# Kernel tuning notes

Hardware: AMD Instinct MI355X
Metric: run time of the kernel (lower is better)

## Reference

```python
import jax, jax.numpy as jnp
import numpy as np
import math

PHI = (1 + math.sqrt(5)) / 2
PI = math.pi
B, N, T, D, H = 2, 16, 512, 512, 8
DH = D // H
HALF = DH // 2
FF = int(D * PHI)  # 828
DC = D
PR_EPS = 1e-8
LN_EPS = 1e-5


def _ln(x, g, b):
    # x: (B,N,T,D); g,b: (N,D)
    mu = x.mean(axis=-1, keepdims=True)
    var = ((x - mu) ** 2).mean(axis=-1, keepdims=True)
    return (x - mu) * jax.lax.rsqrt(var + LN_EPS) * g[None, :, None, :] + b[None, :, None, :]


def _phase_resonance(a, b):
    # a, b: (B, N, D) in fp32; adjacent feature pairs = (re, im)
    pairs = a.shape[-1] // 2
    def to_phase(x):
        x2 = x.reshape(*x.shape[:-1], pairs, 2)
        return jnp.arctan2(x2[..., 1] + PR_EPS, x2[..., 0] + PR_EPS)
    ta, tb = to_phase(a), to_phase(b)
    delta = ta[..., :, None, :] - tb[..., None, :, :]  # (B, N, N, pairs)
    return jnp.cos(delta).mean(axis=-1)                # (B, N, N) in [-1, 1]


def setup_inputs():
    key = jax.random.key(0)
    ks = iter(jax.random.split(key, 24))
    w = lambda shape: jax.random.normal(next(ks), shape, jnp.float32) * 0.02
    return {
        'x': jax.random.normal(next(ks), (B, N, T, D), jnp.float32),
        'gate_w': w((N, D)),
        'gate_b': jnp.full((N,), 2.0, jnp.float32),  # torch init: bias=2.0
        'ln1_g': jnp.ones((N, D), jnp.float32),
        'ln1_b': jnp.zeros((N, D), jnp.float32),
        'wq': w((N, D, D)), 'wk': w((N, D, D)), 'wv': w((N, D, D)), 'wo': w((N, D, D)),
        'phase_angles': jnp.tile(jnp.linspace(0.0, PI, H, dtype=jnp.float32), (N, 1)),
        'ln2_g': jnp.ones((N, D), jnp.float32),
        'ln2_b': jnp.zeros((N, D), jnp.float32),
        'up_w': w((N, D, FF)), 'up_b': jnp.zeros((N, FF), jnp.float32),
        'down_w': w((N, FF, D)), 'down_b': jnp.zeros((N, D), jnp.float32),
        'commit_w': w((N, D)), 'commit_b': jnp.zeros((N,), jnp.float32),
        'center_w': w((N, D, DC)), 'center_b': jnp.zeros((N, DC), jnp.float32),
        'field_in_w': w((D, D)),
        'field_out_w': w((D, D)),
        'conductance': jnp.float32(1.0),
    }


def reference(x, gate_w, gate_b, ln1_g, ln1_b, wq, wk, wv, wo, phase_angles,
              ln2_g, ln2_b, up_w, up_b, down_w, down_b, commit_w, commit_b,
              center_w, center_b, field_in_w, field_out_w, conductance):
    # ---- BinaryAperture (straight-through binary gate) ----
    logits = jnp.einsum('bntd,nd->bnt', x, gate_w) + gate_b[None, :, None]
    prob = jax.nn.sigmoid(logits)  # temperature = 1.0
    hard = (prob > 0.5).astype(x.dtype)
    gate = (hard + prob - jax.lax.stop_gradient(prob))[..., None]  # (B,N,T,1)

    # ---- Field: phase-rotated, gated attention (scores forced to fp32) ----
    h = _ln(x, ln1_g, ln1_b)
    def proj(wm):
        z = jnp.einsum('bntd,nde->bnte', h, wm)
        return z.reshape(B, N, T, H, DH).transpose(0, 1, 3, 2, 4)  # (B,N,H,T,DH)
    Q, K, V = proj(wq), proj(wk), proj(wv)
    cos_a = jnp.cos(phase_angles)[None, :, :, None, None]  # (1,N,H,1,1)
    sin_a = jnp.sin(phase_angles)[None, :, :, None, None]
    def rot(Z):
        re, im = Z[..., :HALF], Z[..., HALF:2 * HALF]
        return jnp.concatenate([re * cos_a - im * sin_a, re * sin_a + im * cos_a], axis=-1)
    Q, K = rot(Q), rot(K)
    ge = gate[:, :, None]  # (B,N,1,T,1) broadcast over heads
    Q = Q * ge
    K = K * ge
    scores = jnp.einsum('bnhtd,bnhsd->bnhts', Q.astype(jnp.float32), K.astype(jnp.float32)) / math.sqrt(DH)
    attn = jax.nn.softmax(scores, axis=-1).astype(V.dtype)
    field = jnp.einsum('bnhts,bnhsd->bnhtd', attn, V)
    field = field.transpose(0, 1, 3, 2, 4).reshape(B, N, T, D)
    field = jnp.einsum('bntd,nde->bnte', field, wo) * gate
    x = x + field

    # ---- Boundary: golden-ratio FFN gated by commit * gate ----
    h2 = _ln(x, ln2_g, ln2_b)
    up = jax.nn.gelu(jnp.einsum('bntd,ndf->bntf', h2, up_w) + up_b[None, :, None], approximate=False)
    ff = jnp.einsum('bntf,nfd->bntd', up, down_w) + down_b[None, :, None]
    center_pool = x.mean(axis=2)  # (B,N,D) (pooled pre-FFN, as in torch)
    commit = jax.nn.sigmoid(jnp.einsum('bnd,nd->bn', center_pool, commit_w) + commit_b[None])  # (B,N)
    x = x + commit[..., None, None] * gate * ff
    center = jnp.tanh(jnp.einsum('bnd,nde->bne', center_pool, center_w) + center_b[None])  # (B,N,DC)

    # ---- SharedField: phase-resonance coupling across the N nodes ----
    node_gates = commit[..., None]  # (B,N,1)
    transmitted = center * node_gates
    h_res = jnp.einsum('bnd,de->bne', center, field_in_w).astype(jnp.float32)
    r_acc = _phase_resonance(h_res, h_res)  # (B,N,N); r_acc None -> r_acc_new = r_instant
    h_tx = jnp.einsum('bnd,de->bne', transmitted, field_in_w)
    recv = conductance * jnp.einsum('bmn,bnd->bmd', r_acc.astype(x.dtype), h_tx)
    field_signal = jnp.einsum('bnd,de->bne', recv, field_out_w)  # (B,N,D)

    # each node's boundary receives the field signal
    return x + field_signal[:, :, None, :]
```

## Files before the change

### kernel.cpp

```cpp
#include <hip/hip_runtime.h>

typedef unsigned short u16;
typedef __attribute__((ext_vector_type(8))) short short8;
typedef __attribute__((ext_vector_type(4))) float f32x4;

#define B_ 2
#define N_ 16
#define T_ 512
#define D_ 512
#define H_ 8
#define DH_ 64
#define HALF_ 32
#define FF_ 828
#define FFP_ 832
#define DC_ 512
#define LN_EPS 1e-5f
#define PR_EPS 1e-8f
#define NEG_INF (-3.0e38f)

__device__ __forceinline__ float b2f(u16 u) { return __uint_as_float(((unsigned)u) << 16); }
__device__ __forceinline__ u16 f2b(float f) {
  unsigned x = __float_as_uint(f);
  return (u16)((x + 0x7fffu + ((x >> 16) & 1u)) >> 16);
}
__device__ __forceinline__ float gelu_exact(float z) {
  return 0.5f * z * (1.f + erff(z * 0.70710678118654752f));
}

typedef __attribute__((address_space(1))) const unsigned GASu;
typedef __attribute__((address_space(3))) unsigned LASu;
__device__ __forceinline__ void gload_lds16(const void* g, void* l) {
  __builtin_amdgcn_global_load_lds((GASu*)g, (LASu*)l, 16, 0, 0);
}

__global__ __launch_bounds__(256) void ln_gate_kernel(
    const float* __restrict__ xsrc,
    const float* __restrict__ gate_w, const float* __restrict__ gate_b,
    const float* __restrict__ lng, const float* __restrict__ lnb,
    float* __restrict__ gate_out, u16* __restrict__ h_out, int do_gate) {
  __shared__ float redA[4], redB[4], redC[4];
  int bnt = blockIdx.x;
  int n = (bnt / T_) % N_;
  int tid = threadIdx.x;
  int lane = tid & 63, wave = tid >> 6;
  const float* xr = xsrc + (size_t)bnt * D_;
  float x0 = xr[tid], x1 = xr[tid + 256];
  float s = x0 + x1;
  #pragma unroll
  for (int off = 32; off > 0; off >>= 1) s += __shfl_xor(s, off);
  if (lane == 0) redA[wave] = s;
  if (do_gate) {
    float t = x0 * gate_w[n * D_ + tid] + x1 * gate_w[n * D_ + tid + 256];
    #pragma unroll
    for (int off = 32; off > 0; off >>= 1) t += __shfl_xor(t, off);
    if (lane == 0) redC[wave] = t;
  }
  __syncthreads();
  float mu = (redA[0] + redA[1] + redA[2] + redA[3]) * (1.f / D_);
  float d0 = x0 - mu, d1 = x1 - mu;
  float v = d0 * d0 + d1 * d1;
  #pragma unroll
  for (int off = 32; off > 0; off >>= 1) v += __shfl_xor(v, off);
  if (lane == 0) redB[wave] = v;
  __syncthreads();
  float rstd = rsqrtf((redB[0] + redB[1] + redB[2] + redB[3]) * (1.f / D_) + LN_EPS);
  if (do_gate && tid == 0)
    gate_out[bnt] = (redC[0] + redC[1] + redC[2] + redC[3] + gate_b[n] > 0.f) ? 1.f : 0.f;
  size_t o = (size_t)bnt * D_;
  h_out[o + tid]       = f2b(d0 * rstd * lng[n * D_ + tid]       + lnb[n * D_ + tid]);
  h_out[o + tid + 256] = f2b(d1 * rstd * lng[n * D_ + tid + 256] + lnb[n * D_ + tid + 256]);
}

__global__ __launch_bounds__(256) void wconv_kernel(
    const float* __restrict__ W, u16* __restrict__ Wt, int Kd, int E, int Kpad) {
  __shared__ u16 tile[32][33];
  int e0 = blockIdx.x * 32, k0 = blockIdx.y * 32, n = blockIdx.z;
  const float* Wb = W + (size_t)n * Kd * E;
  u16* Wtb = Wt + (size_t)n * E * Kpad;
  int r = threadIdx.x >> 3, c4 = (threadIdx.x & 7) * 4;
  int kk = k0 + r;
  if (kk < Kd) {
    if (e0 + c4 + 3 < E) {
      float4 w4 = *(const float4*)(Wb + (size_t)kk * E + e0 + c4);
      tile[r][c4 + 0] = f2b(w4.x); tile[r][c4 + 1] = f2b(w4.y);
      tile[r][c4 + 2] = f2b(w4.z); tile[r][c4 + 3] = f2b(w4.w);
    } else {
      #pragma unroll
      for (int j = 0; j < 4; ++j) {
        int ee = e0 + c4 + j;
        tile[r][c4 + j] = (ee < E) ? f2b(Wb[(size_t)kk * E + ee]) : (u16)0;
      }
    }
  } else {
    #pragma unroll
    for (int j = 0; j < 4; ++j) tile[r][c4 + j] = 0;
  }
  __syncthreads();
  int ee = e0 + r;
  if (ee < E) {
    u16* dst = Wtb + (size_t)ee * Kpad + k0 + c4;
    if (k0 + c4 + 3 < Kpad) {
      ushort4 o;
      o.x = tile[c4 + 0][r]; o.y = tile[c4 + 1][r];
      o.z = tile[c4 + 2][r]; o.w = tile[c4 + 3][r];
      *(ushort4*)dst = o;
    } else {
      #pragma unroll
      for (int j = 0; j < 4; ++j) if (k0 + c4 + j < Kpad) dst[j] = tile[c4 + j][r];
    }
  }
}

__global__ __launch_bounds__(256) void vtrans_kernel(const u16* __restrict__ V, u16* __restrict__ Vt) {
  __shared__ u16 tile[32][36];
  int tt0 = blockIdx.x * 32;
  int dd0 = blockIdx.y * 32;
  int bh = blockIdx.z;
  int bn = bh >> 3, h = bh & 7;
  const u16* src = V + (size_t)bn * T_ * D_ + h * DH_;
  int r = threadIdx.x >> 3, c4 = (threadIdx.x & 7) * 4;
  *(ushort4*)&tile[r][c4] = *(const ushort4*)(src + (size_t)(tt0 + r) * D_ + dd0 + c4);
  __syncthreads();
  u16* dst = Vt + ((size_t)bh * DH_ + dd0 + r) * T_ + tt0 + c4;
  ushort4 o;
  o.x = tile[c4 + 0][r]; o.y = tile[c4 + 1][r];
  o.z = tile[c4 + 2][r]; o.w = tile[c4 + 3][r];
  *(ushort4*)dst = o;
}

#define BM 128
#define BN 128
#define BK 64
__global__ __launch_bounds__(256) void gemm_mfma_kernel(
    const u16* __restrict__ In,
    const float* __restrict__ W0, const float* __restrict__ W1, const float* __restrict__ W2,
    const u16* __restrict__ Wt0, const u16* __restrict__ Wt1, const u16* __restrict__ Wt2,
    u16* __restrict__ O0, u16* __restrict__ O1, u16* __restrict__ O2,
    float* __restrict__ OutF,
    int Kd, int KdW, int E, int Es, int mode,
    const float* __restrict__ bias,
    const float* __restrict__ xres, const float* __restrict__ gate) {
  __shared__ __align__(16) u16 As[BM * BK];
  __shared__ __align__(16) u16 Bs[BN * BK];
  int z = blockIdx.z;
  int bn = z & 31, proj = z >> 5;
  int n = bn & (N_ - 1);
  const float* W = (proj == 0) ? W0 : ((proj == 1) ? W1 : W2);
  const u16* Wt = (proj == 0) ? Wt0 : ((proj == 1) ? Wt1 : Wt2);
  u16* Out = (proj == 0) ? O0 : ((proj == 1) ? O1 : O2);
  int e0 = blockIdx.x * BN, t0 = blockIdx.y * BM;
  int tid = threadIdx.x;
  int lane = tid & 63, wave = tid >> 6;
  int m_off = (wave & 1) * 64, n_off = (wave >> 1) * 64;
  int ml = lane & 15, quad = lane >> 4;
  const u16* Inb = In + (size_t)bn * T_ * Kd;
  const float* Wb = W ? W + (size_t)n * (size_t)KdW * E : nullptr;
  const u16* Wtb = Wt ? Wt + (size_t)n * E * Kd : nullptr;

  int lrow = lane >> 3;
  int lchunk = ((lane & 7) ^ lrow) * 8;

  f32x4 acc[4][4] = {};

  int ksteps = (Kd + BK - 1) / BK;
  for (int ks = 0; ks < ksteps; ++ks) {
    int k0 = ks * BK;
    if (Wtb) {
      #pragma unroll
      for (int it = 0; it < 4; ++it) {
        int r0 = wave * 32 + it * 8;
        gload_lds16(Inb + (size_t)(t0 + r0 + lrow) * Kd + k0 + lchunk, &As[r0 * BK]);
        gload_lds16(Wtb + (size_t)(e0 + r0 + lrow) * Kd + k0 + lchunk, &Bs[r0 * BK]);
      }
    } else {
      #pragma unroll
      for (int it = 0; it < 4; ++it) {
        int cid = tid * 4 + it;
        int r = cid >> 3, cp = cid & 7;
        int clog = cp ^ (r & 7);
        int kg = k0 + clog * 8;
        u16* dst = &As[r * BK + cp * 8];
        const u16* src = Inb + (size_t)(t0 + r) * Kd + kg;
        if (kg + 8 <= Kd) {
          *(short8*)dst = *(const short8*)src;
        } else {
          #pragma unroll
          for (int xx = 0; xx < 8; ++xx) dst[xx] = (kg + xx < Kd) ? src[xx] : (u16)0;
        }
        int eg = e0 + r;
        u16* bdst = &Bs[r * BK + cp * 8];
        #pragma unroll
        for (int xx = 0; xx < 8; ++xx)
          bdst[xx] = (kg + xx < KdW && eg < E) ? f2b(Wb[(size_t)(kg + xx) * E + eg]) : (u16)0;
      }
    }
    __syncthreads();
    #pragma unroll
    for (int kst = 0; kst < 2; ++kst) {
      int so = ((kst * 4 + quad) ^ (ml & 7)) * 8;
      short8 a[4], b[4];
      #pragma unroll
      for (int i = 0; i < 4; ++i)
        a[i] = *(const short8*)&As[(m_off + i * 16 + ml) * BK + so];
      #pragma unroll
      for (int j = 0; j < 4; ++j)
        b[j] = *(const short8*)&Bs[(n_off + j * 16 + ml) * BK + so];
      #pragma unroll
      for (int i = 0; i < 4; ++i)
        #pragma unroll
        for (int j = 0; j < 4; ++j)
          acc[i][j] = __builtin_amdgcn_mfma_f32_16x16x32_bf16(a[i], b[j], acc[i][j], 0, 0, 0);
    }
    __syncthreads();
  }

  #pragma unroll
  for (int j = 0; j < 4; ++j) {
    int eg = e0 + n_off + j * 16 + ml;
    if (eg >= Es) continue;
    #pragma unroll
    for (int i = 0; i < 4; ++i) {
      #pragma unroll
      for (int r = 0; r < 4; ++r) {
        int tg = t0 + m_off + i * 16 + quad * 4 + r;
        float v = acc[i][j][r];
        size_t o = (size_t)bn * T_ * Es + (size_t)tg * Es + eg;
        if (mode == 0) {
          Out[o] = f2b(v);
        } else if (mode == 1) {
          float g = gate[(size_t)bn * T_ + tg];
          OutF[o] = xres[o] + v * g;
        } else if (mode == 2) {
          Out[o] = (eg < E) ? f2b(gelu_exact(v + bias[(size_t)n * E + eg])) : (u16)0;
        } else {
          Out[o] = f2b(v + bias[(size_t)n * E + eg]);
        }
      }
    }
  }
}

__global__ __launch_bounds__(256) void rot_gate_kernel(
    u16* __restrict__ q, u16* __restrict__ k,
    const float* __restrict__ phase, const float* __restrict__ gate) {
  long long i = (long long)blockIdx.x * 256 + threadIdx.x;
  int c = (int)(i & 31);
  int h = (int)((i >> 5) & 7);
  int t = (int)((i >> 8) & 511);
  int bn = (int)(i >> 17);
  int n = bn & (N_ - 1);
  float a = phase[n * H_ + h];
  float ca = cosf(a), sa = sinf(a);
  float g = gate[(size_t)bn * T_ + t];
  size_t base = ((size_t)bn * T_ + t) * D_ + h * DH_;
  float qr = b2f(q[base + c]), qi = b2f(q[base + c + HALF_]);
  u16 a0 = f2b((qr * ca - qi * sa) * g);
  u16 a1 = f2b((qr * sa + qi * ca) * g);
  q[base + c]         = f2b(b2f(a0) * 0.125f);
  q[base + c + HALF_] = f2b(b2f(a1) * 0.125f);
  float kr = b2f(k[base + c]), ki = b2f(k[base + c + HALF_]);
  k[base + c]         = f2b((kr * ca - ki * sa) * g);
  k[base + c + HALF_] = f2b((kr * sa + ki * ca) * g);
}

#define ATS 72
__global__ __launch_bounds__(256) void attn_kernel(
    const u16* __restrict__ Q, const u16* __restrict__ K, const u16* __restrict__ V,
    const u16* __restrict__ Vt, u16* __restrict__ O) {
  __shared__ __align__(16) u16 Qs[64 * ATS];
  __shared__ __align__(16) u16 Ks[64 * ATS];
  __shared__ __align__(16) u16 Vs[64 * ATS];
  __shared__ __align__(16) u16 Ps[64 * ATS];
  int qt = blockIdx.x, h = blockIdx.y, bn = blockIdx.z;
  int tid = threadIdx.x;
  int lane = tid & 63, wave = tid >> 6;
  int ml = lane & 15, quad = lane >> 4;
  int t0 = qt * 64;
  size_t rowbase = (size_t)bn * T_ * D_ + (size_t)h * DH_;
  int r = tid >> 2;
  int c = (tid & 3) * 16;

  {
    const u16* src = Q + rowbase + (size_t)(t0 + r) * D_ + c;
    *(short8*)&Qs[r * ATS + c]     = *(const short8*)(src);
    *(short8*)&Qs[r * ATS + c + 8] = *(const short8*)(src + 8);
  }
  const u16* ksrc = K + rowbase + (size_t)r * D_ + c;
  const u16* vsrc = Vt ? (Vt + ((size_t)(bn * H_ + h) * DH_ + r) * T_ + c) : nullptr;

  float m_[4], l_[4];
  f32x4 acco[4] = {};
  #pragma unroll
  for (int rr = 0; rr < 4; ++rr) { m_[rr] = NEG_INF; l_[rr] = 0.f; }

  for (int sc = 0; sc < 8; ++sc) {
    int s0 = sc * 64;
    {
      const u16* kp = ksrc + (size_t)s0 * D_;
      *(short8*)&Ks[r * ATS + c]     = *(const short8*)(kp);
      *(short8*)&Ks[r * ATS + c + 8] = *(const short8*)(kp + 8);
    }
    if (Vt) {
      const u16* vp = vsrc + s0;
      *(short8*)&Vs[r * ATS + c]     = *(const short8*)(vp);
      *(short8*)&Vs[r * ATS + c + 8] = *(const short8*)(vp + 8);
    } else {
      int sw = wave * 16;
      const u16* src = V + rowbase + (size_t)(s0 + sw) * D_ + lane;
      short8 v0, v1;
      #pragma unroll
      for (int rr = 0; rr < 8; ++rr) ((u16*)&v0)[rr] = src[(size_t)rr * D_];
      #pragma unroll
      for (int rr = 0; rr < 8; ++rr) ((u16*)&v1)[rr] = src[(size_t)(rr + 8) * D_];
      *(short8*)&Vs[lane * ATS + sw]     = v0;
      *(short8*)&Vs[lane * ATS + sw + 8] = v1;
    }
    __syncthreads();

    f32x4 s4[4] = {};
    #pragma unroll
    for (int kst = 0; kst < 2; ++kst) {
      short8 a = *(const short8*)&Qs[(wave * 16 + ml) * ATS + kst * 32 + quad * 8];
      #pragma unroll
      for (int j = 0; j < 4; ++j) {
        short8 b = *(const short8*)&Ks[(j * 16 + ml) * ATS + kst * 32 + quad * 8];
        s4[j] = __builtin_amdgcn_mfma_f32_16x16x32_bf16(a, b, s4[j], 0, 0, 0);
      }
    }

    #pragma unroll
    for (int rr = 0; rr < 4; ++rr) {
      float cm = fmaxf(fmaxf(s4[0][rr], s4[1][rr]), fmaxf(s4[2][rr], s4[3][rr]));
      #pragma unroll
      for (int off = 1; off < 16; off <<= 1) cm = fmaxf(cm, __shfl_xor(cm, off));
      if (cm > m_[rr]) {
        float al = __expf(m_[rr] - cm);
        l_[rr] *= al;
        #pragma unroll
        for (int jd = 0; jd < 4; ++jd) acco[jd][rr] *= al;
        m_[rr] = cm;
      }
      u16 q0 = f2b(__expf(s4[0][rr] - m_[rr])), q1 = f2b(__expf(s4[1][rr] - m_[rr]));
      u16 q2 = f2b(__expf(s4[2][rr] - m_[rr])), q3 = f2b(__expf(s4[3][rr] - m_[rr]));
      float rs = b2f(q0) + b2f(q1) + b2f(q2) + b2f(q3);
      #pragma unroll
      for (int off = 1; off < 16; off <<= 1) rs += __shfl_xor(rs, off);
      l_[rr] += rs;
      int trow = wave * 16 + quad * 4 + rr;
      Ps[trow * ATS + 0 * 16 + ml] = q0;
      Ps[trow * ATS + 1 * 16 + ml] = q1;
      Ps[trow * ATS + 2 * 16 + ml] = q2;
      Ps[trow * ATS + 3 * 16 + ml] = q3;
    }

    #pragma unroll
    for (int sst = 0; sst < 2; ++sst) {
      short8 a = *(const short8*)&Ps[(wave * 16 + ml) * ATS + sst * 32 + quad * 8];
      #pragma unroll
      for (int jd = 0; jd < 4; ++jd) {
        short8 b = *(const short8*)&Vs[(jd * 16 + ml) * ATS + sst * 32 + quad * 8];
        acco[jd] = __builtin_amdgcn_mfma_f32_16x16x32_bf16(a, b, acco[jd], 0, 0, 0);
      }
    }
    __syncthreads();
  }

  #pragma unroll
  for (int rr = 0; rr < 4; ++rr) {
    float inv = 1.f / l_[rr];
    int trow = t0 + wave * 16 + quad * 4 + rr;
    #pragma unroll
    for (int jd = 0; jd < 4; ++jd)
      O[rowbase + (size_t)trow * D_ + jd * 16 + ml] = f2b(acco[jd][rr] * inv);
  }
}

__global__ __launch_bounds__(256) void pool1_kernel(const float* __restrict__ x2, float* __restrict__ part) {
  int tc = blockIdx.x & 15, bn = blockIdx.x >> 4;
  int d = threadIdx.x;
  const float* base = x2 + ((size_t)bn * T_ + tc * 32) * D_;
  float s0 = 0.f, s1 = 0.f;
  for (int t = 0; t < 32; ++t) {
    s0 += base[(size_t)t * D_ + d];
    s1 += base[(size_t)t * D_ + d + 256];
  }
  float* p = part + ((size_t)bn * 16 + tc) * D_;
  p[d] = s0; p[d + 256] = s1;
}
__global__ __launch_bounds__(256) void pool2_kernel(const float* __restrict__ part, float* __restrict__ cp) {
  int bn = blockIdx.x;
  int d = threadIdx.x;
  float s0 = 0.f, s1 = 0.f;
  for (int tc = 0; tc < 16; ++tc) {
    s0 += part[((size_t)bn * 16 + tc) * D_ + d];
    s1 += part[((size_t)bn * 16 + tc) * D_ + d + 256];
  }
  cp[(size_t)bn * D_ + d]       = s0 * (1.f / T_);
  cp[(size_t)bn * D_ + d + 256] = s1 * (1.f / T_);
}

__global__ __launch_bounds__(256) void commit_center_kernel(
    const float* __restrict__ cp, const float* __restrict__ commit_w, const float* __restrict__ commit_b,
    const float* __restrict__ center_w, const float* __restrict__ center_b,
    float* __restrict__ commit, float* __restrict__ center) {
  __shared__ float cps[512];
  __shared__ float red[256];
  int bn = blockIdx.x, n = bn % N_, tid = threadIdx.x;
  cps[tid] = cp[(size_t)bn * D_ + tid];
  cps[tid + 256] = cp[(size_t)bn * D_ + tid + 256];
  __syncthreads();
  red[tid] = cps[tid] * commit_w[n * D_ + tid] + cps[tid + 256] * commit_w[n * D_ + tid + 256];
  __syncthreads();
  for (int s = 128; s > 0; s >>= 1) { if (tid < s) red[tid] += red[tid + s]; __syncthreads(); }
  if (tid == 0) commit[bn] = 1.f / (1.f + expf(-(red[0] + commit_b[n])));
  #pragma unroll
  for (int eo = 0; eo < 2; ++eo) {
    int e = eo * 256 + tid;
    float acc = center_b[(size_t)n * DC_ + e];
    for (int d = 0; d < D_; ++d) acc = fmaf(cps[d], center_w[((size_t)n * D_ + d) * DC_ + e], acc);
    center[(size_t)bn * DC_ + e] = tanhf(acc);
  }
}

__global__ __launch_bounds__(256) void matvec_kernel(
    const float* __restrict__ inp, const float* __restrict__ Wm, float* __restrict__ outp) {
  __shared__ float s[512];
  int bn = blockIdx.x, tid = threadIdx.x;
  s[tid] = inp[(size_t)bn * D_ + tid];
  s[tid + 256] = inp[(size_t)bn * D_ + tid + 256];
  __syncthreads();
  #pragma unroll
  for (int eo = 0; eo < 2; ++eo) {
    int e = eo * 256 + tid;
    float acc = 0.f;
    for (int d = 0; d < D_; ++d) acc = fmaf(s[d], Wm[(size_t)d * D_ + e], acc);
    outp[(size_t)bn * D_ + e] = acc;
  }
}

__global__ __launch_bounds__(256) void uv_kernel(
    const float* __restrict__ hres, float* __restrict__ u, float* __restrict__ v) {
  int i = blockIdx.x * 256 + threadIdx.x;
  float xr = hres[2 * i] + PR_EPS;
  float yi = hres[2 * i + 1] + PR_EPS;
  float r = sqrtf(xr * xr + yi * yi);
  u[i] = xr / r; v[i] = yi / r;
}

__global__ __launch_bounds__(256) void racc_kernel(
    const float* __restrict__ u, const float* __restrict__ v, float* __restrict__ ra) {
  int b = blockIdx.x, tid = threadIdx.x;
  int mm = tid >> 4, nn = tid & 15;
  const float* ub = u + (size_t)b * N_ * 256;
  const float* vb = v + (size_t)b * N_ * 256;
  float acc = 0.f;
  for (int p = 0; p < 256; ++p)
    acc += ub[mm * 256 + p] * ub[nn * 256 + p] + vb[mm * 256 + p] * vb[nn * 256 + p];
  ra[(size_t)b * N_ * N_ + mm * N_ + nn] = acc * (1.f / 256.f);
}

__global__ __launch_bounds__(256) void recv_kernel(
    const float* __restrict__ ra, const float* __restrict__ commit,
    const float* __restrict__ hres, const float* __restrict__ cond, float* __restrict__ recv) {
  int bn = blockIdx.x, b = bn / N_, mm = bn % N_, tid = threadIdx.x;
  float c = cond[0];
  #pragma unroll
  for (int eo = 0; eo < 2; ++eo) {
    int d = eo * 256 + tid;
    float acc = 0.f;
    for (int nn = 0; nn < N_; ++nn)
      acc += ra[(size_t)b * N_ * N_ + mm * N_ + nn] * commit[b * N_ + nn] *
             hres[((size_t)b * N_ + nn) * D_ + d];
    recv[(size_t)bn * D_ + d] = c * acc;
  }
}

__global__ __launch_bounds__(256) void final_kernel(
    const float* __restrict__ x2, const float* __restrict__ commit,
    const float* __restrict__ gate, const u16* __restrict__ ff,
    const float* __restrict__ fs, float* __restrict__ out) {
  long long i4 = (long long)blockIdx.x * 256 + threadIdx.x;
  long long base = i4 * 4;
  int d = (int)(base & (D_ - 1));
  int t = (int)((base >> 9) & (T_ - 1));
  int bn = (int)(base >> 18);
  float cg = commit[bn] * gate[(size_t)bn * T_ + t];
  float4 xv = *(const float4*)(x2 + base);
  ushort4 fv = *(const ushort4*)(ff + base);
  float4 sv = *(const float4*)(fs + (size_t)bn * D_ + d);
  float4 r;
  r.x = xv.x + cg * b2f(fv.x) + sv.x;
  r.y = xv.y + cg * b2f(fv.y) + sv.y;
  r.z = xv.z + cg * b2f(fv.z) + sv.z;
  r.w = xv.w + cg * b2f(fv.w) + sv.w;
  *(float4*)(out + base) = r;
}

extern "C" void kernel_launch(void* const* d_in, const int* in_sizes, int n_in,
                              void* d_out, int out_size, void* d_ws, size_t ws_size,
                              hipStream_t stream) {
  (void)in_sizes; (void)n_in; (void)out_size;
  const float* x          = (const float*)d_in[0];
  const float* gate_w     = (const float*)d_in[1];
  const float* gate_b     = (const float*)d_in[2];
  const float* ln1_g      = (const float*)d_in[3];
  const float* ln1_b      = (const float*)d_in[4];
  const float* wq         = (const float*)d_in[5];
  const float* wk         = (const float*)d_in[6];
  const float* wv         = (const float*)d_in[7];
  const float* wo         = (const float*)d_in[8];
  const float* phase      = (const float*)d_in[9];
  const float* ln2_g      = (const float*)d_in[10];
  const float* ln2_b      = (const float*)d_in[11];
  const float* up_w       = (const float*)d_in[12];
  const float* up_b       = (const float*)d_in[13];
  const float* down_w     = (const float*)d_in[14];
  const float* down_b     = (const float*)d_in[15];
  const float* commit_w   = (const float*)d_in[16];
  const float* commit_b   = (const float*)d_in[17];
  const float* center_w   = (const float*)d_in[18];
  const float* center_b   = (const float*)d_in[19];
  const float* field_in_w = (const float*)d_in[20];
  const float* field_out_w= (const float*)d_in[21];
  const float* cond       = (const float*)d_in[22];

  const long long BNTD = 8388608LL;
  u16* w16 = (u16*)d_ws;
  u16* R0 = w16;
  u16* R1 = w16 + BNTD;
  u16* R2 = w16 + 2 * BNTD;
  u16* R3 = w16 + 3 * BNTD;
  float* sm   = (float*)(w16 + 4 * BNTD);
  float* gate   = sm;
  float* cp     = sm + 16384;
  float* center = sm + 2 * 16384;
  float* hres   = sm + 3 * 16384;
  float* uu     = sm + 4 * 16384;
  float* vv     = uu + 8192;
  float* ra     = vv + 8192;
  float* recvb  = ra + 512;
  float* fsig   = recvb + 16384;
  float* commit = fsig + 16384;
  float* part   = sm + 115232;
  float* x2 = (float*)d_out;

  const size_t WSQ = (size_t)N_ * 512 * 512;
  const size_t WUPu = (size_t)N_ * 828 * 512;
  const size_t WUPd = (size_t)N_ * 512 * 832;
  u16* wtbase = (u16*)(sm + 115232 + 262144);
  u16* wtq = wtbase;
  u16* wtk = wtq + WSQ;
  u16* wtv = wtk + WSQ;
  u16* wto = wtv + WSQ;
  u16* wtu = wto + WSQ;
  u16* wtd = wtu + WUPu;
  u16* vtb = wtd + WUPd;
  size_t needed = (size_t)((char*)(vtb + BNTD) - (char*)d_ws);
  bool use_wt = ws_size >= needed;

  ln_gate_kernel<<<16384, 256, 0, stream>>>(x, gate_w, gate_b, ln1_g, ln1_b, gate, R0, 1);

  if (use_wt) {
    wconv_kernel<<<dim3(16, 16, 16), 256, 0, stream>>>(wq, wtq, 512, 512, 512);
    wconv_kernel<<<dim3(16, 16, 16), 256, 0, stream>>>(wk, wtk, 512, 512, 512);
    wconv_kernel<<<dim3(16, 16, 16), 256, 0, stream>>>(wv, wtv, 512, 512, 512);
    wconv_kernel<<<dim3(16, 16, 16), 256, 0, stream>>>(wo, wto, 512, 512, 512);
    wconv_kernel<<<dim3(26, 16, 16), 256, 0, stream>>>(up_w, wtu, 512, 828, 512);
    wconv_kernel<<<dim3(16, 26, 16), 256, 0, stream>>>(down_w, wtd, 828, 512, 832);
  }
  const u16* pq = use_wt ? wtq : nullptr;
  const u16* pk = use_wt ? wtk : nullptr;
  const u16* pv = use_wt ? wtv : nullptr;
  const u16* po = use_wt ? wto : nullptr;
  const u16* pu = use_wt ? wtu : nullptr;
  const u16* pd = use_wt ? wtd : nullptr;

  gemm_mfma_kernel<<<dim3(4, 4, 96), 256, 0, stream>>>(
      R0, wq, wk, wv, pq, pk, pv, R1, R2, R3, nullptr,
      512, 512, 512, 512, 0, nullptr, nullptr, nullptr);
  rot_gate_kernel<<<16384, 256, 0, stream>>>(R1, R2, phase, gate);
  if (use_wt) vtrans_kernel<<<dim3(16, 2, 256), 256, 0, stream>>>(R3, vtb);
  attn_kernel<<<dim3(8, 8, 32), 256, 0, stream>>>(R1, R2, R3, use_wt ? vtb : nullptr, R0);
  gemm_mfma_kernel<<<dim3(4, 4, 32), 256, 0, stream>>>(
      R0, wo, nullptr, nullptr, po, nullptr, nullptr, nullptr, nullptr, nullptr, x2,
      512, 512, 512, 512, 1, nullptr, x, gate);
  ln_gate_kernel<<<16384, 256, 0, stream>>>(x2, nullptr, nullptr, ln2_g, ln2_b, nullptr, R1, 0);
  gemm_mfma_kernel<<<dim3(7, 4, 32), 256, 0, stream>>>(
      R1, up_w, nullptr, nullptr, pu, nullptr, nullptr, R2, nullptr, nullptr, nullptr,
      512, 512, 828, 832, 2, up_b, nullptr, nullptr);
  gemm_mfma_kernel<<<dim3(4, 4, 32), 256, 0, stream>>>(
      R2, down_w, nullptr, nullptr, pd, nullptr, nullptr, R0, nullptr, nullptr, nullptr,
      832, 828, 512, 512, 3, down_b, nullptr, nullptr);
  pool1_kernel<<<512, 256, 0, stream>>>(x2, part);
  pool2_kernel<<<32, 256, 0, stream>>>(part, cp);
  commit_center_kernel<<<32, 256, 0, stream>>>(cp, commit_w, commit_b, center_w, center_b, commit, center);
  matvec_kernel<<<32, 256, 0, stream>>>(center, field_in_w, hres);
  uv_kernel<<<32, 256, 0, stream>>>(hres, uu, vv);
  racc_kernel<<<2, 256, 0, stream>>>(uu, vv, ra);
  recv_kernel<<<32, 256, 0, stream>>>(ra, commit, hres, cond, recvb);
  matvec_kernel<<<32, 256, 0, stream>>>(recvb, field_out_w, fsig);
  final_kernel<<<8192, 256, 0, stream>>>(x2, commit, gate, R0, fsig, x2);
}
```

Measured before the change: 780.4 us.

## Fuse rotary phase gating into QKV GEMM epilogue and remap blocks per XCD

The separate rot_gate kernel is removed and its rotation, gating and q-scaling are applied in the QKV GEMM epilogue. Each wave's 64 output columns form one head, so the re/im halves are acc[j] and acc[j+2]. This avoids a full read-modify-write pass over Q and K. All GEMM launches also move to a 1D grid that keeps each z-slice's tiles on one XCD (blockIdx & 7), to improve L2 reuse of the weights and inputs. The bf16 rounding sequence is kept so results match, at the cost of a larger epilogue.

```diff
diff --git a/kernel.cpp b/kernel.cpp
--- a/kernel.cpp
+++ b/kernel.cpp
@@ -139,16 +139,22 @@
     float* __restrict__ OutF,
     int Kd, int KdW, int E, int Es, int mode,
     const float* __restrict__ bias,
-    const float* __restrict__ xres, const float* __restrict__ gate) {
+    const float* __restrict__ xres, const float* __restrict__ gate,
+    const float* __restrict__ phase, int doRot,
+    int xdim, int nXY, int zPerXcd) {
   __shared__ __align__(16) u16 As[BM * BK];
   __shared__ __align__(16) u16 Bs[BN * BK];
-  int z = blockIdx.z;
+  int L = blockIdx.x;
+  int xcd = L & 7, slot = L >> 3;
+  int zloc = slot / nXY, xy = slot - zloc * nXY;
+  int z = xcd * zPerXcd + zloc;
+  int bx = xy % xdim, by = xy / xdim;
   int bn = z & 31, proj = z >> 5;
   int n = bn & (N_ - 1);
   const float* W = (proj == 0) ? W0 : ((proj == 1) ? W1 : W2);
   const u16* Wt = (proj == 0) ? Wt0 : ((proj == 1) ? Wt1 : Wt2);
   u16* Out = (proj == 0) ? O0 : ((proj == 1) ? O1 : O2);
-  int e0 = blockIdx.x * BN, t0 = blockIdx.y * BM;
+  int e0 = bx * BN, t0 = by * BM;
   int tid = threadIdx.x;
   int lane = tid & 63, wave = tid >> 6;
   int m_off = (wave & 1) * 64, n_off = (wave >> 1) * 64;
@@ -214,53 +220,57 @@
     __syncthreads();
   }
 
-  #pragma unroll
-  for (int j = 0; j < 4; ++j) {
-    int eg = e0 + n_off + j * 16 + ml;
-    if (eg >= Es) continue;
+  int rmode = doRot ? ((proj == 0) ? 2 : ((proj == 1) ? 1 : 0)) : 0;
+  if (rmode) {
+    int h = (e0 + n_off) >> 6;
+    float ang = phase[n * H_ + h];
+    float ca = cosf(ang), sa = sinf(ang);
     #pragma unroll
     for (int i = 0; i < 4; ++i) {
       #pragma unroll
       for (int r = 0; r < 4; ++r) {
         int tg = t0 + m_off + i * 16 + quad * 4 + r;
-        float v = acc[i][j][r];
-        size_t o = (size_t)bn * T_ * Es + (size_t)tg * Es + eg;
-        if (mode == 0) {
-          Out[o] = f2b(v);
-        } else if (mode == 1) {
-          float g = gate[(size_t)bn * T_ + tg];
-          OutF[o] = xres[o] + v * g;
-        } else if (mode == 2) {
-          Out[o] = (eg < E) ? f2b(gelu_exact(v + bias[(size_t)n * E + eg])) : (u16)0;
-        } else {
-          Out[o] = f2b(v + bias[(size_t)n * E + eg]);
+        float g = gate[(size_t)bn * T_ + tg];
+        #pragma unroll
+        for (int j = 0; j < 2; ++j) {
+          int eg = e0 + n_off + j * 16 + ml;
+          size_t o = (size_t)bn * T_ * Es + (size_t)tg * Es + eg;
+          float re = b2f(f2b(acc[i][j][r]));
+          float im = b2f(f2b(acc[i][j + 2][r]));
+          u16 a0 = f2b((re * ca - im * sa) * g);
+          u16 a1 = f2b((re * sa + im * ca) * g);
+          if (rmode == 2) { a0 = f2b(b2f(a0) * 0.125f); a1 = f2b(b2f(a1) * 0.125f); }
+          Out[o] = a0;
+          Out[o + 32] = a1;
         }
       }
     }
-  }
-}
-
-__global__ __launch_bounds__(256) void rot_gate_kernel(
-    u16* __restrict__ q, u16* __restrict__ k,
-    const float* __restrict__ phase, const float* __restrict__ gate) {
-  long long i = (long long)blockIdx.x * 256 + threadIdx.x;
-  int c = (int)(i & 31);
-  int h = (int)((i >> 5) & 7);
-  int t = (int)((i >> 8) & 511);
-  int bn = (int)(i >> 17);
-  int n = bn & (N_ - 1);
-  float a = phase[n * H_ + h];
-  float ca = cosf(a), sa = sinf(a);
-  float g = gate[(size_t)bn * T_ + t];
-  size_t base = ((size_t)bn * T_ + t) * D_ + h * DH_;
-  float qr = b2f(q[base + c]), qi = b2f(q[base + c + HALF_]);
-  u16 a0 = f2b((qr * ca - qi * sa) * g);
-  u16 a1 = f2b((qr * sa + qi * ca) * g);
-  q[base + c]         = f2b(b2f(a0) * 0.125f);
-  q[base + c + HALF_] = f2b(b2f(a1) * 0.125f);
-  float kr = b2f(k[base + c]), ki = b2f(k[base + c + HALF_]);
-  k[base + c]         = f2b((kr * ca - ki * sa) * g);
-  k[base + c + HALF_] = f2b((kr * sa + ki * ca) * g);
+  } else {
+    #pragma unroll
+    for (int j = 0; j < 4; ++j) {
+      int eg = e0 + n_off + j * 16 + ml;
+      if (eg >= Es) continue;
+      #pragma unroll
+      for (int i = 0; i < 4; ++i) {
+        #pragma unroll
+        for (int r = 0; r < 4; ++r) {
+          int tg = t0 + m_off + i * 16 + quad * 4 + r;
+          float v = acc[i][j][r];
+          size_t o = (size_t)bn * T_ * Es + (size_t)tg * Es + eg;
+          if (mode == 0) {
+            Out[o] = f2b(v);
+          } else if (mode == 1) {
+            float g = gate[(size_t)bn * T_ + tg];
+            OutF[o] = xres[o] + v * g;
+          } else if (mode == 2) {
+            Out[o] = (eg < E) ? f2b(gelu_exact(v + bias[(size_t)n * E + eg])) : (u16)0;
+          } else {
+            Out[o] = f2b(v + bias[(size_t)n * E + eg]);
+          }
+        }
+      }
+    }
+  }
 }
 
 #define ATS 72
@@ -575,22 +585,21 @@
   const u16* pu = use_wt ? wtu : nullptr;
   const u16* pd = use_wt ? wtd : nullptr;
 
-  gemm_mfma_kernel<<<dim3(4, 4, 96), 256, 0, stream>>>(
+  gemm_mfma_kernel<<<1536, 256, 0, stream>>>(
       R0, wq, wk, wv, pq, pk, pv, R1, R2, R3, nullptr,
-      512, 512, 512, 512, 0, nullptr, nullptr, nullptr);
-  rot_gate_kernel<<<16384, 256, 0, stream>>>(R1, R2, phase, gate);
+      512, 512, 512, 512, 0, nullptr, nullptr, gate, phase, 1, 4, 16, 12);
   if (use_wt) vtrans_kernel<<<dim3(16, 2, 256), 256, 0, stream>>>(R3, vtb);
   attn_kernel<<<dim3(8, 8, 32), 256, 0, stream>>>(R1, R2, R3, use_wt ? vtb : nullptr, R0);
-  gemm_mfma_kernel<<<dim3(4, 4, 32), 256, 0, stream>>>(
+  gemm_mfma_kernel<<<512, 256, 0, stream>>>(
       R0, wo, nullptr, nullptr, po, nullptr, nullptr, nullptr, nullptr, nullptr, x2,
-      512, 512, 512, 512, 1, nullptr, x, gate);
+      512, 512, 512, 512, 1, nullptr, x, gate, nullptr, 0, 4, 16, 4);
   ln_gate_kernel<<<16384, 256, 0, stream>>>(x2, nullptr, nullptr, ln2_g, ln2_b, nullptr, R1, 0);
-  gemm_mfma_kernel<<<dim3(7, 4, 32), 256, 0, stream>>>(
+  gemm_mfma_kernel<<<896, 256, 0, stream>>>(
       R1, up_w, nullptr, nullptr, pu, nullptr, nullptr, R2, nullptr, nullptr, nullptr,
-      512, 512, 828, 832, 2, up_b, nullptr, nullptr);
-  gemm_mfma_kernel<<<dim3(4, 4, 32), 256, 0, stream>>>(
+      512, 512, 828, 832, 2, up_b, nullptr, nullptr, nullptr, 0, 7, 28, 4);
+  gemm_mfma_kernel<<<512, 256, 0, stream>>>(
       R2, down_w, nullptr, nullptr, pd, nullptr, nullptr, R0, nullptr, nullptr, nullptr,
-      832, 828, 512, 512, 3, down_b, nullptr, nullptr);
+      832, 828, 512, 512, 3, down_b, nullptr, nullptr, nullptr, 0, 4, 16, 4);
   pool1_kernel<<<512, 256, 0, stream>>>(x2, part);
   pool2_kernel<<<32, 256, 0, stream>>>(part, cp);
   commit_center_kernel<<<32, 256, 0, stream>>>(cp, commit_w, commit_b, center_w, center_b, commit, center);
```

After: 743.3 us. 1.05x faster.
